# Optimization experiments

Hardware: AMD Instinct MI355X
Metric: run time of the kernel (lower is better)

Reference implementation:

```python
import jax, jax.numpy as jnp
import numpy as np

L_MODES = 64
GRID = 128
OUT_GRID = 128
CIN = 64
COUT = 64
T_DIM = 256


def legendre_table(L, theta):
    """Fully-normalized associated Legendre P_bar_l^m(cos(theta)), Condon-Shortley.
    Returns (L, 2L-1, n_theta) with m indexed -(L-1)..(L-1) at axis 1."""
    nt = theta.shape[0]
    x = np.cos(theta)
    s = np.sin(theta)
    P = np.zeros((L, L, nt))
    P[0, 0] = np.sqrt(1.0 / (4.0 * np.pi))
    for m in range(1, L):
        P[m, m] = -np.sqrt((2.0 * m + 1.0) / (2.0 * m)) * s * P[m - 1, m - 1]
    for m in range(L - 1):
        P[m + 1, m] = np.sqrt(2.0 * m + 3.0) * x * P[m, m]
    for m in range(L):
        for l in range(m + 2, L):
            a = np.sqrt((4.0 * l * l - 1.0) / (l * l - m * m))
            b = np.sqrt(((l - 1.0) ** 2 - m * m) / (4.0 * (l - 1.0) ** 2 - 1.0))
            P[l, m] = a * (x * P[l - 1, m] - b * P[l - 2, m])
    T = np.zeros((L, 2 * L - 1, nt))
    for m in range(L):
        T[:, L - 1 + m, :] = P[:, m, :]
        if m > 0:
            T[:, L - 1 - m, :] = ((-1.0) ** m) * P[:, m, :]
    return T.astype(np.float32)


def setup_inputs() -> dict:
    key = jax.random.key(0)
    ks = jax.random.split(key, 8)
    theta = np.pi * (np.arange(GRID) + 0.5) / GRID
    theta_out = np.pi * (np.arange(OUT_GRID) + 0.5) / OUT_GRID
    P_in = jnp.asarray(legendre_table(L_MODES, theta))            # (L, 2L-1, GRID)
    P_out = jnp.asarray(legendre_table(L_MODES, theta_out))       # (L, 2L-1, OUT_GRID)
    quad_w = jnp.asarray((np.pi / GRID) * np.sin(theta), dtype=jnp.float32)
    scale_w = 1.0 / (CIN + COUT)
    return {
        "x": jax.random.normal(ks[0], (GRID, GRID, CIN), jnp.float32),
        "t_emb": jax.random.normal(ks[1], (T_DIM,), jnp.float32),
        "wr": scale_w * jax.random.normal(ks[2], (L_MODES, 2 * L_MODES - 1, CIN, COUT), jnp.float32),
        "wi": scale_w * jax.random.normal(ks[3], (L_MODES, 2 * L_MODES - 1, CIN, COUT), jnp.float32),
        "conv_w": jax.random.normal(ks[4], (CIN, COUT), jnp.float32) / np.sqrt(CIN),
        "conv_b": jnp.zeros((COUT,), jnp.float32),
        "time_w": jax.random.normal(ks[5], (COUT, COUT), jnp.float32),
        "dense_w": jax.random.normal(ks[6], (T_DIM, 2 * COUT), jnp.float32) / np.sqrt(T_DIM),
        "ln_scale": jnp.ones((COUT,), jnp.float32),
        "ln_bias": jnp.zeros((COUT,), jnp.float32),
        "P_in": P_in,
        "P_out": P_out,
        "quad_w": quad_w,
    }


def reference(x, t_emb, wr, wi, conv_w, conv_b, time_w, dense_w, ln_scale, ln_bias, P_in, P_out, quad_w):
    L = P_in.shape[0]
    G_out = P_out.shape[2]
    nlon = x.shape[1]
    m_idx = np.arange(-(L - 1), L)

    # ---- forward spherical harmonic transform (lon FFT + Legendre quadrature) ----
    f = jnp.fft.fft(x.astype(jnp.complex64), axis=1) * (2.0 * np.pi / nlon)  # (nlat, nlon, Cin)
    fm = f[:, np.mod(m_idx, nlon), :] * quad_w[:, None, None]                # (nlat, 2L-1, Cin)
    flm = jnp.einsum('tmc,lmt->lmc', fm, P_in)                                # (L, 2L-1, Cin)

    # ---- per-(l,m) complex spectral conv ----
    w = wr + 1j * wi
    flm = jnp.einsum('lmi,lmio->lmo', flm, w)                                 # (L, 2L-1, Cout)

    # ---- inverse SHT onto output grid ----
    g = jnp.einsum('lmo,lmt->tmo', flm, P_out)                                # (G_out, 2L-1, Cout)
    phi = 2.0 * np.pi * np.arange(G_out) / G_out
    E = jnp.asarray(np.exp(1j * np.outer(m_idx, phi)).astype(np.complex64))   # (2L-1, G_out)
    x_spec = jnp.real(jnp.einsum('tmo,mk->tko', g, E))                        # (G_out, G_out, Cout)

    # ---- residual time-conditioned path (TimeConv2D, einsum as written in source) ----
    h = jnp.einsum('lmk,ko->lmo', x, conv_w) + conv_b                          # 1x1 conv
    psi = t_emb @ dense_w
    w_t, b_t = jnp.split(psi, 2, axis=-1)
    h = jnp.einsum('ij,j,lmk->lmi', time_w, w_t, h) + b_t[None, None, :]
    h = jax.image.resize(h, (G_out, G_out, h.shape[-1]), method='bicubic')

    # ---- add, layernorm over channels, relu ----
    out = x_spec + h
    mu = jnp.mean(out, axis=-1, keepdims=True)
    var = jnp.var(out, axis=-1, keepdims=True)
    out = (out - mu) * jax.lax.rsqrt(var + 1e-6) * ln_scale + ln_bias
    return jax.nn.relu(out)
```

## Files before the change

### kernel.cpp

```cpp
#include <hip/hip_runtime.h>
#include <math.h>

#define LM 64
#define MM 127
#define GG 128
#define CC 64
#define OO 64

#define TWO_PI 6.28318530717958647692f

__global__ __launch_bounds__(256) void k_dft(const float* __restrict__ x,
                                             const float* __restrict__ quad_w,
                                             const float* __restrict__ conv_w,
                                             const float* __restrict__ conv_b,
                                             const float* __restrict__ t_emb,
                                             const float* __restrict__ dense_w,
                                             const float* __restrict__ time_w,
                                             float2* __restrict__ F,
                                             float* __restrict__ Sv,
                                             float* __restrict__ aux) {
    int b = blockIdx.x;
    int tx = threadIdx.x;

    if (b == 512) {
        __shared__ float psis[128];
        if (tx < 128) {
            float acc = 0.f;
            for (int tq = 0; tq < 256; ++tq) acc += t_emb[tq] * dense_w[tq * 128 + tx];
            psis[tx] = acc;
            aux[tx] = acc;
        }
        __syncthreads();
        if (tx < 64) {
            float tv = 0.f;
            for (int q = 0; q < 64; ++q) tv += time_w[tx * 64 + q] * psis[q];
            aux[128 + tx] = tv;
        }
        return;
    }

    int t = b >> 2, cq = b & 3;
    int c0base = cq * 16;

    __shared__ __align__(16) float xs[GG * 16];
    __shared__ float2 tab[GG];
    __shared__ float cwsl[16];
    __shared__ float Sp[2][GG];
    __shared__ float bsum_s;

    {
        const float* xp = x + (size_t)t * GG * CC + c0base;
        for (int idx = tx; idx < GG * 16 / 4; idx += 256) {
            int n = idx >> 2, c4 = idx & 3;
            *(float4*)&xs[n * 16 + c4 * 4] = *(const float4*)&xp[n * CC + c4 * 4];
        }
    }
    if (tx < GG) {
        float ang = (TWO_PI / GG) * tx;
        tab[tx] = make_float2(cosf(ang), sinf(ang));
    }
    if (tx >= 128 && tx < 144) {
        int c = c0base + (tx - 128);
        float s = 0.f;
        for (int o = 0; o < OO; ++o) s += conv_w[c * OO + o];
        cwsl[tx - 128] = s;
    }
    if (tx == 144) {
        float bs = 0.f;
        for (int o = 0; o < OO; ++o) bs += conv_b[o];
        bsum_s = bs;
    }
    __syncthreads();

    int k = tx & 63, cg = tx >> 6;
    int c0 = cg * 4;

    float sr[4], si[4];
#pragma unroll
    for (int j = 0; j < 4; ++j) { sr[j] = 0.f; si[j] = 0.f; }

    int kn = 0;
#pragma unroll 4
    for (int n = 0; n < GG; ++n) {
        float2 w = tab[kn];
        const float4 v = *(const float4*)&xs[n * 16 + c0];
        float vv[4] = {v.x, v.y, v.z, v.w};
#pragma unroll
        for (int j = 0; j < 4; ++j) {
            sr[j] += vv[j] * w.x;
            si[j] -= vv[j] * w.y;
        }
        kn = (kn + k) & (GG - 1);
    }
    float sc = (TWO_PI / GG) * quad_w[t];

    {
        float2* Fp = F + ((size_t)t * 64 + k) * CC + c0base + c0;
        *(float4*)&Fp[0] = make_float4(sr[0] * sc, si[0] * sc, sr[1] * sc, si[1] * sc);
        *(float4*)&Fp[2] = make_float4(sr[2] * sc, si[2] * sc, sr[3] * sc, si[3] * sc);
    }

    {
        int n2 = tx & 127, h = tx >> 7;
        float p = 0.f;
#pragma unroll
        for (int j = 0; j < 8; ++j) p += xs[n2 * 16 + h * 8 + j] * cwsl[h * 8 + j];
        Sp[h][n2] = p;
    }
    __syncthreads();
    if (tx < GG) {
        float v = Sp[0][tx] + Sp[1][tx] + (cq == 0 ? bsum_s : 0.f);
        Sv[(size_t)cq * GG * GG + t * GG + tx] = v;
    }
}

__global__ __launch_bounds__(256) void k_leg_fwd(const float2* __restrict__ F,
                                                 const float* __restrict__ P_in,
                                                 float2* __restrict__ flmp) {
    int m = blockIdx.x;
    int lh = blockIdx.y;
    int tq = blockIdx.z;
    int l0 = lh * 32;
    if (l0 + 31 < m) return;
    int t0 = tq * 32;

    __shared__ __align__(16) float2 Fs[32 * 64];
    __shared__ __align__(16) float  Ps[32 * 36];
    int tx = threadIdx.x;
    int c = tx & 63, lg = tx >> 6;

    for (int idx = tx; idx < 32 * 32; idx += 256) {
        int lr = idx >> 5, tl = idx & 31;
        Ps[tl * 36 + lr] = P_in[((size_t)(l0 + lr) * MM + 63 + m) * GG + t0 + tl];
    }
    for (int idx = tx; idx < 32 * 64; idx += 256) {
        int tl = idx >> 6, cc = idx & 63;
        Fs[idx] = F[((size_t)(t0 + tl) * 64 + m) * CC + cc];
    }
    __syncthreads();

    float sr[8], si[8];
#pragma unroll
    for (int j = 0; j < 8; ++j) { sr[j] = 0.f; si[j] = 0.f; }

#pragma unroll 2
    for (int tl = 0; tl < 32; ++tl) {
        float2 f = Fs[tl * 64 + c];
        const float* pp = &Ps[tl * 36 + lg * 8];
        float4 p0 = *(const float4*)pp;
        float4 p1 = *(const float4*)(pp + 4);
        float pv[8] = {p0.x, p0.y, p0.z, p0.w, p1.x, p1.y, p1.z, p1.w};
#pragma unroll
        for (int j = 0; j < 8; ++j) {
            sr[j] += f.x * pv[j];
            si[j] += f.y * pv[j];
        }
    }
#pragma unroll
    for (int j = 0; j < 8; ++j) {
        int l = l0 + lg * 8 + j;
        if (l >= m)
            flmp[(((size_t)tq * 64 + l) * 64 + m) * CC + c] = make_float2(sr[j], si[j]);
    }
}

__global__ __launch_bounds__(256) void k_wmul(const float2* __restrict__ flmp,
                                              const float* __restrict__ wr,
                                              const float* __restrict__ wi,
                                              float2* __restrict__ flm2) {
    int l = blockIdx.x, mi = blockIdx.y;
    int m = mi - 63;
    int am = m < 0 ? -m : m;
    if (l < am) return;
    __shared__ float2 fs[CC];
    __shared__ float2 part[16][CC];
    int tx = threadIdx.x, ol = tx & 15, ig = tx >> 4;
    if (tx < 64) {
        float2 f = make_float2(0.f, 0.f);
#pragma unroll
        for (int q = 0; q < 4; ++q) {
            float2 v = flmp[(((size_t)q * 64 + l) * 64 + am) * CC + tx];
            f.x += v.x;
            f.y += v.y;
        }
        if (m < 0) {
            float sgn = (am & 1) ? -1.f : 1.f;
            f.x *= sgn;
            f.y *= -sgn;
        }
        fs[tx] = f;
    }
    __syncthreads();
    size_t base = ((size_t)(l * MM + mi) * CC) * OO;
    const float4* wr4 = (const float4*)(wr + base);
    const float4* wi4 = (const float4*)(wi + base);
    float ar[4] = {0.f, 0.f, 0.f, 0.f}, ai[4] = {0.f, 0.f, 0.f, 0.f};
#pragma unroll
    for (int di = 0; di < 4; ++di) {
        int i = ig * 4 + di;
        float4 a = wr4[i * 16 + ol];
        float4 b = wi4[i * 16 + ol];
        float2 f = fs[i];
        ar[0] += f.x * a.x - f.y * b.x;  ai[0] += f.x * b.x + f.y * a.x;
        ar[1] += f.x * a.y - f.y * b.y;  ai[1] += f.x * b.y + f.y * a.y;
        ar[2] += f.x * a.z - f.y * b.z;  ai[2] += f.x * b.z + f.y * a.z;
        ar[3] += f.x * a.w - f.y * b.w;  ai[3] += f.x * b.w + f.y * a.w;
    }
#pragma unroll
    for (int j = 0; j < 4; ++j) part[ig][ol * 4 + j] = make_float2(ar[j], ai[j]);
    __syncthreads();
    if (tx < 64) {
        float rr = 0.f, ri = 0.f;
#pragma unroll
        for (int q = 0; q < 16; ++q) {
            float2 p = part[q][tx];
            rr += p.x;
            ri += p.y;
        }
        flm2[(size_t)(l * MM + mi) * OO + tx] = make_float2(rr, ri);
    }
}

__global__ __launch_bounds__(256) void k_leg_inv(const float2* __restrict__ flm2,
                                                 const float* __restrict__ P_out,
                                                 float2* __restrict__ g) {
    int mi = blockIdx.x;
    int th = blockIdx.y >> 1, oh = blockIdx.y & 1;
    int t0 = th * 32, o0 = oh * 32;

    __shared__ __align__(16) float2 Ws[64 * 32];
    __shared__ __align__(16) float  Ps[64 * 32];
    int tx = threadIdx.x;
    int ol = tx & 31, tg = tx >> 5;
    int o = o0 + ol;

    for (int idx = tx; idx < 64 * 32; idx += 256) {
        int ls = idx >> 5, oo = idx & 31;
        Ws[idx] = flm2[(size_t)(ls * MM + mi) * OO + o0 + oo];
    }
    for (int idx = tx; idx < 64 * 32; idx += 256) {
        int ls = idx >> 5, tt = idx & 31;
        Ps[idx] = P_out[((size_t)ls * MM + mi) * GG + t0 + tt];
    }
    __syncthreads();

    float gr[4], gi[4];
#pragma unroll
    for (int j = 0; j < 4; ++j) { gr[j] = 0.f; gi[j] = 0.f; }

#pragma unroll 2
    for (int l = 0; l < 64; ++l) {
        float2 wv = Ws[l * 32 + ol];
        const float4 p = *(const float4*)&Ps[l * 32 + tg * 4];
        float pv[4] = {p.x, p.y, p.z, p.w};
#pragma unroll
        for (int j = 0; j < 4; ++j) {
            gr[j] += wv.x * pv[j];
            gi[j] += wv.y * pv[j];
        }
    }
#pragma unroll
    for (int j = 0; j < 4; ++j) {
        int t = t0 + tg * 4 + j;
        g[((size_t)t * MM + mi) * OO + o] = make_float2(gr[j], gi[j]);
    }
}

__global__ __launch_bounds__(512) void k_final(const float2* __restrict__ g,
                                               const float* __restrict__ Sv,
                                               const float* __restrict__ aux,
                                               const float* __restrict__ ln_scale,
                                               const float* __restrict__ ln_bias,
                                               float* __restrict__ out) {
    __shared__ float2 gs[64 * 64];
    __shared__ float Ss[64];
    int t = blockIdx.x, kh = blockIdx.y;
    int tx = threadIdx.x;
    int o = tx & 63, kg = tx >> 6;

    if (tx < 64) {
        float s = 0.f;
#pragma unroll
        for (int q = 0; q < 4; ++q) s += Sv[(size_t)q * GG * GG + t * GG + kh * 64 + tx];
        Ss[tx] = s;
    }

    float zr[8], zi[8], accr[8], acci[8];
#pragma unroll
    for (int j = 0; j < 8; ++j) {
        int k = kh * 64 + kg * 8 + j;
        float phi = (TWO_PI / GG) * k;
        float s, c;
        sincosf(phi, &s, &c);
        zr[j] = c; zi[j] = s;
        accr[j] = 0.f; acci[j] = 0.f;
    }

    for (int pass = 0; pass < 2; ++pass) {
        int mbase = (pass == 0) ? 64 : 0;
        int cnt = (pass == 0) ? 63 : 64;
        __syncthreads();
        for (int idx = tx; idx < cnt * 64; idx += 512) {
            int mm = idx >> 6, oo = idx & 63;
            gs[idx] = g[((size_t)t * MM + mbase + mm) * OO + oo];
        }
        __syncthreads();
        for (int mm = cnt - 1; mm >= 0; --mm) {
            float2 gv = gs[mm * 64 + o];
#pragma unroll
            for (int j = 0; j < 8; ++j) {
                float tr = accr[j] * zr[j] - acci[j] * zi[j] + gv.x;
                float ti = accr[j] * zi[j] + acci[j] * zr[j] + gv.y;
                accr[j] = tr; acci[j] = ti;
            }
        }
    }

    float tvec = aux[128 + o], bt = aux[64 + o];
    float lns = ln_scale[o], lnb = ln_bias[o];
#pragma unroll
    for (int j = 0; j < 8; ++j) {
        int k = kh * 64 + kg * 8 + j;
        float sgn = (k & 1) ? -1.f : 1.f;
        float xsp = sgn * (accr[j] * zr[j] - acci[j] * zi[j]);
        float val = xsp + tvec * Ss[k - kh * 64] + bt;

        float mu = val;
#pragma unroll
        for (int off = 1; off < 64; off <<= 1) mu += __shfl_xor(mu, off);
        mu *= (1.f / 64.f);
        float d = val - mu;
        float var = d * d;
#pragma unroll
        for (int off = 1; off < 64; off <<= 1) var += __shfl_xor(var, off);
        var *= (1.f / 64.f);
        float r = d * rsqrtf(var + 1e-6f) * lns + lnb;
        out[((size_t)(t * GG) + k) * OO + o] = fmaxf(r, 0.f);
    }
}

extern "C" void kernel_launch(void* const* d_in, const int* in_sizes, int n_in,
                              void* d_out, int out_size, void* d_ws, size_t ws_size,
                              hipStream_t stream) {
    const float* x        = (const float*)d_in[0];
    const float* t_emb    = (const float*)d_in[1];
    const float* wr       = (const float*)d_in[2];
    const float* wi       = (const float*)d_in[3];
    const float* conv_w   = (const float*)d_in[4];
    const float* conv_b   = (const float*)d_in[5];
    const float* time_w   = (const float*)d_in[6];
    const float* dense_w  = (const float*)d_in[7];
    const float* ln_scale = (const float*)d_in[8];
    const float* ln_bias  = (const float*)d_in[9];
    const float* P_in     = (const float*)d_in[10];
    const float* P_out    = (const float*)d_in[11];
    const float* quad_w   = (const float*)d_in[12];

    float* ws = (float*)d_ws;
    float*  aux  = ws;
    float2* F    = (float2*)(ws + 512);
    float2* flmp = (float2*)(ws + 1049088);
    float2* flm2 = (float2*)(ws + 3146240);
    float2* g    = (float2*)(ws + 4186624);
    float*  Sv   = ws + 6267392;

    float* out = (float*)d_out;

    k_dft<<<513, 256, 0, stream>>>(x, quad_w, conv_w, conv_b, t_emb, dense_w, time_w,
                                   F, Sv, aux);
    k_leg_fwd<<<dim3(64, 2, 4), 256, 0, stream>>>(F, P_in, flmp);
    k_wmul<<<dim3(LM, MM), 256, 0, stream>>>(flmp, wr, wi, flm2);
    k_leg_inv<<<dim3(MM, 8), 256, 0, stream>>>(flm2, P_out, g);
    k_final<<<dim3(GG, 2), 512, 0, stream>>>(g, Sv, aux, ln_scale, ln_bias, out);
}
```

Measured before the change: 325.5 us.

## Fuse five stage kernels into one cooperative persistent kernel with grid syncs

Merges the DFT, forward Legendre, weight multiply, inverse Legendre and final layernorm kernels into one cooperative kernel of 512 blocks separated by grid.sync, with a shared-memory union reused across stages. Stages that had more or fewer blocks now use grid-stride loops, and the final stage is remapped to 256 threads per block over quarter k-ranges. The aim is to remove the per-launch overhead and the gaps between the five launches. The cost is serialized grid barriers, a fixed grid size that leaves large stages such as the weight multiply to loop, and a reduced thread count in the final stage. Skipped weight-multiply tiles now write explicit zeros, which the previous version did not do.

```diff
diff --git a/kernel.cpp b/kernel.cpp
--- a/kernel.cpp
+++ b/kernel.cpp
@@ -1,341 +1,334 @@
 #include <hip/hip_runtime.h>
+#include <hip/hip_cooperative_groups.h>
 #include <math.h>
+
+namespace cg = cooperative_groups;
 
 #define LM 64
 #define MM 127
 #define GG 128
 #define CC 64
 #define OO 64
+#define NBLK 512
 
 #define TWO_PI 6.28318530717958647692f
 
-__global__ __launch_bounds__(256) void k_dft(const float* __restrict__ x,
-                                             const float* __restrict__ quad_w,
-                                             const float* __restrict__ conv_w,
-                                             const float* __restrict__ conv_b,
-                                             const float* __restrict__ t_emb,
-                                             const float* __restrict__ dense_w,
-                                             const float* __restrict__ time_w,
-                                             float2* __restrict__ F,
-                                             float* __restrict__ Sv,
-                                             float* __restrict__ aux) {
+__global__ __launch_bounds__(256, 2) void k_fused(
+    const float* __restrict__ x, const float* __restrict__ t_emb,
+    const float* __restrict__ wr, const float* __restrict__ wi,
+    const float* __restrict__ conv_w, const float* __restrict__ conv_b,
+    const float* __restrict__ time_w, const float* __restrict__ dense_w,
+    const float* __restrict__ ln_scale, const float* __restrict__ ln_bias,
+    const float* __restrict__ P_in, const float* __restrict__ P_out,
+    const float* __restrict__ quad_w,
+    float2* __restrict__ F, float2* __restrict__ flmp,
+    float2* __restrict__ flm2, float2* __restrict__ g,
+    float* __restrict__ Sv, float* __restrict__ aux,
+    float* __restrict__ out)
+{
+    cg::grid_group grid = cg::this_grid();
     int b = blockIdx.x;
     int tx = threadIdx.x;
 
-    if (b == 512) {
-        __shared__ float psis[128];
-        if (tx < 128) {
-            float acc = 0.f;
-            for (int tq = 0; tq < 256; ++tq) acc += t_emb[tq] * dense_w[tq * 128 + tx];
-            psis[tx] = acc;
-            aux[tx] = acc;
-        }
-        __syncthreads();
-        if (tx < 64) {
-            float tv = 0.f;
-            for (int q = 0; q < 64; ++q) tv += time_w[tx * 64 + q] * psis[q];
-            aux[128 + tx] = tv;
-        }
-        return;
-    }
-
-    int t = b >> 2, cq = b & 3;
-    int c0base = cq * 16;
-
-    __shared__ __align__(16) float xs[GG * 16];
-    __shared__ float2 tab[GG];
-    __shared__ float cwsl[16];
-    __shared__ float Sp[2][GG];
-    __shared__ float bsum_s;
+    __shared__ __align__(16) union {
+        struct { float xs[GG * 16]; float2 tab[GG]; float cwsl[16];
+                 float Sp[2][GG]; float bsum; } p1;
+        float psis[128];
+        struct { float2 Fs[32 * 64]; float Ps[32 * 36]; } p2;
+        struct { float2 fs[CC]; float2 part[16][CC]; } p3;
+        struct { float2 Ws[64 * 32]; float Ps[64 * 32]; } p4;
+        struct { float2 gs[64 * 64]; float Ss[32]; } p5;
+    } u;
 
     {
+        int t = b >> 2, cq = b & 3;
+        int c0base = cq * 16;
+
         const float* xp = x + (size_t)t * GG * CC + c0base;
         for (int idx = tx; idx < GG * 16 / 4; idx += 256) {
             int n = idx >> 2, c4 = idx & 3;
-            *(float4*)&xs[n * 16 + c4 * 4] = *(const float4*)&xp[n * CC + c4 * 4];
-        }
-    }
-    if (tx < GG) {
-        float ang = (TWO_PI / GG) * tx;
-        tab[tx] = make_float2(cosf(ang), sinf(ang));
-    }
-    if (tx >= 128 && tx < 144) {
-        int c = c0base + (tx - 128);
-        float s = 0.f;
-        for (int o = 0; o < OO; ++o) s += conv_w[c * OO + o];
-        cwsl[tx - 128] = s;
-    }
-    if (tx == 144) {
-        float bs = 0.f;
-        for (int o = 0; o < OO; ++o) bs += conv_b[o];
-        bsum_s = bs;
-    }
-    __syncthreads();
-
-    int k = tx & 63, cg = tx >> 6;
-    int c0 = cg * 4;
-
-    float sr[4], si[4];
-#pragma unroll
-    for (int j = 0; j < 4; ++j) { sr[j] = 0.f; si[j] = 0.f; }
-
-    int kn = 0;
+            *(float4*)&u.p1.xs[n * 16 + c4 * 4] = *(const float4*)&xp[n * CC + c4 * 4];
+        }
+        if (tx < GG) {
+            float ang = (TWO_PI / GG) * tx;
+            u.p1.tab[tx] = make_float2(cosf(ang), sinf(ang));
+        }
+        if (tx >= 128 && tx < 144) {
+            int c = c0base + (tx - 128);
+            float s = 0.f;
+            for (int o = 0; o < OO; ++o) s += conv_w[c * OO + o];
+            u.p1.cwsl[tx - 128] = s;
+        }
+        if (tx == 144) {
+            float bs = 0.f;
+            for (int o = 0; o < OO; ++o) bs += conv_b[o];
+            u.p1.bsum = bs;
+        }
+        __syncthreads();
+
+        int k = tx & 63, cgrp = tx >> 6;
+        int c0 = cgrp * 4;
+
+        float sr[4], si[4];
+#pragma unroll
+        for (int j = 0; j < 4; ++j) { sr[j] = 0.f; si[j] = 0.f; }
+
+        int kn = 0;
 #pragma unroll 4
-    for (int n = 0; n < GG; ++n) {
-        float2 w = tab[kn];
-        const float4 v = *(const float4*)&xs[n * 16 + c0];
-        float vv[4] = {v.x, v.y, v.z, v.w};
+        for (int n = 0; n < GG; ++n) {
+            float2 w = u.p1.tab[kn];
+            const float4 v = *(const float4*)&u.p1.xs[n * 16 + c0];
+            float vv[4] = {v.x, v.y, v.z, v.w};
+#pragma unroll
+            for (int j = 0; j < 4; ++j) {
+                sr[j] += vv[j] * w.x;
+                si[j] -= vv[j] * w.y;
+            }
+            kn = (kn + k) & (GG - 1);
+        }
+        float sc = (TWO_PI / GG) * quad_w[t];
+        {
+            float2* Fp = F + ((size_t)t * 64 + k) * CC + c0base + c0;
+            *(float4*)&Fp[0] = make_float4(sr[0] * sc, si[0] * sc, sr[1] * sc, si[1] * sc);
+            *(float4*)&Fp[2] = make_float4(sr[2] * sc, si[2] * sc, sr[3] * sc, si[3] * sc);
+        }
+
+        {
+            int n2 = tx & 127, h = tx >> 7;
+            float p = 0.f;
+#pragma unroll
+            for (int j = 0; j < 8; ++j) p += u.p1.xs[n2 * 16 + h * 8 + j] * u.p1.cwsl[h * 8 + j];
+            u.p1.Sp[h][n2] = p;
+        }
+        __syncthreads();
+        if (tx < GG) {
+            float v = u.p1.Sp[0][tx] + u.p1.Sp[1][tx] + (cq == 0 ? u.p1.bsum : 0.f);
+            Sv[(size_t)cq * GG * GG + t * GG + tx] = v;
+        }
+
+        if (b == 0) {
+            __syncthreads();
+            if (tx < 128) {
+                float acc = 0.f;
+                for (int tq = 0; tq < 256; ++tq) acc += t_emb[tq] * dense_w[tq * 128 + tx];
+                u.psis[tx] = acc;
+                aux[tx] = acc;
+            }
+            __syncthreads();
+            if (tx < 64) {
+                float tv = 0.f;
+                for (int q = 0; q < 64; ++q) tv += time_w[tx * 64 + q] * u.psis[q];
+                aux[128 + tx] = tv;
+            }
+        }
+    }
+    grid.sync();
+
+    {
+        int m = b & 63, lh = (b >> 6) & 1, tq = b >> 7;
+        int l0 = lh * 32, t0 = tq * 32;
+        if (l0 + 31 >= m) {
+            int c = tx & 63, lg = tx >> 6;
+
+            for (int idx = tx; idx < 32 * 32; idx += 256) {
+                int lr = idx >> 5, tl = idx & 31;
+                u.p2.Ps[tl * 36 + lr] = P_in[((size_t)(l0 + lr) * MM + 63 + m) * GG + t0 + tl];
+            }
+            for (int idx = tx; idx < 32 * 64; idx += 256) {
+                int tl = idx >> 6, cc = idx & 63;
+                u.p2.Fs[idx] = F[((size_t)(t0 + tl) * 64 + m) * CC + cc];
+            }
+            __syncthreads();
+
+            float sr[8], si[8];
+#pragma unroll
+            for (int j = 0; j < 8; ++j) { sr[j] = 0.f; si[j] = 0.f; }
+
+#pragma unroll 2
+            for (int tl = 0; tl < 32; ++tl) {
+                float2 f = u.p2.Fs[tl * 64 + c];
+                const float* pp = &u.p2.Ps[tl * 36 + lg * 8];
+                float4 p0 = *(const float4*)pp;
+                float4 p1 = *(const float4*)(pp + 4);
+                float pv[8] = {p0.x, p0.y, p0.z, p0.w, p1.x, p1.y, p1.z, p1.w};
+#pragma unroll
+                for (int j = 0; j < 8; ++j) {
+                    sr[j] += f.x * pv[j];
+                    si[j] += f.y * pv[j];
+                }
+            }
+#pragma unroll
+            for (int j = 0; j < 8; ++j) {
+                int l = l0 + lg * 8 + j;
+                if (l >= m)
+                    flmp[(((size_t)tq * 64 + l) * 64 + m) * CC + c] = make_float2(sr[j], si[j]);
+            }
+        }
+    }
+    grid.sync();
+
+    for (int tt = b; tt < 64 * MM; tt += NBLK) {
+        int l = tt / MM, mi = tt % MM;
+        int m = mi - 63;
+        int am = m < 0 ? -m : m;
+        if (l < am) {
+            if (tx < 64) flm2[(size_t)(l * MM + mi) * OO + tx] = make_float2(0.f, 0.f);
+            continue;
+        }
+        int ol = tx & 15, ig = tx >> 4;
+        if (tx < 64) {
+            float2 f = make_float2(0.f, 0.f);
+#pragma unroll
+            for (int q = 0; q < 4; ++q) {
+                float2 v = flmp[(((size_t)q * 64 + l) * 64 + am) * CC + tx];
+                f.x += v.x;
+                f.y += v.y;
+            }
+            if (m < 0) {
+                float sgn = (am & 1) ? -1.f : 1.f;
+                f.x *= sgn;
+                f.y *= -sgn;
+            }
+            u.p3.fs[tx] = f;
+        }
+        __syncthreads();
+        size_t base = ((size_t)(l * MM + mi) * CC) * OO;
+        const float4* wr4 = (const float4*)(wr + base);
+        const float4* wi4 = (const float4*)(wi + base);
+        float ar[4] = {0.f, 0.f, 0.f, 0.f}, ai[4] = {0.f, 0.f, 0.f, 0.f};
+#pragma unroll
+        for (int di = 0; di < 4; ++di) {
+            int i = ig * 4 + di;
+            float4 a = wr4[i * 16 + ol];
+            float4 bb = wi4[i * 16 + ol];
+            float2 f = u.p3.fs[i];
+            ar[0] += f.x * a.x - f.y * bb.x;  ai[0] += f.x * bb.x + f.y * a.x;
+            ar[1] += f.x * a.y - f.y * bb.y;  ai[1] += f.x * bb.y + f.y * a.y;
+            ar[2] += f.x * a.z - f.y * bb.z;  ai[2] += f.x * bb.z + f.y * a.z;
+            ar[3] += f.x * a.w - f.y * bb.w;  ai[3] += f.x * bb.w + f.y * a.w;
+        }
+#pragma unroll
+        for (int j = 0; j < 4; ++j) u.p3.part[ig][ol * 4 + j] = make_float2(ar[j], ai[j]);
+        __syncthreads();
+        if (tx < 64) {
+            float rr = 0.f, ri = 0.f;
+#pragma unroll
+            for (int q = 0; q < 16; ++q) {
+                float2 p = u.p3.part[q][tx];
+                rr += p.x;
+                ri += p.y;
+            }
+            flm2[(size_t)(l * MM + mi) * OO + tx] = make_float2(rr, ri);
+        }
+        __syncthreads();
+    }
+    grid.sync();
+
+    for (int tt = b; tt < MM * 8; tt += NBLK) {
+        int mi = tt % MM, y = tt / MM;
+        int th = y >> 1, oh = y & 1;
+        int t0 = th * 32, o0 = oh * 32;
+        int ol = tx & 31, tg = tx >> 5;
+        int o = o0 + ol;
+
+        __syncthreads();
+        for (int idx = tx; idx < 64 * 32; idx += 256) {
+            int ls = idx >> 5, oo = idx & 31;
+            u.p4.Ws[idx] = flm2[(size_t)(ls * MM + mi) * OO + o0 + oo];
+        }
+        for (int idx = tx; idx < 64 * 32; idx += 256) {
+            int ls = idx >> 5, t2 = idx & 31;
+            u.p4.Ps[idx] = P_out[((size_t)ls * MM + mi) * GG + t0 + t2];
+        }
+        __syncthreads();
+
+        float gr[4], gi[4];
+#pragma unroll
+        for (int j = 0; j < 4; ++j) { gr[j] = 0.f; gi[j] = 0.f; }
+
+#pragma unroll 2
+        for (int l = 0; l < 64; ++l) {
+            float2 wv = u.p4.Ws[l * 32 + ol];
+            const float4 p = *(const float4*)&u.p4.Ps[l * 32 + tg * 4];
+            float pv[4] = {p.x, p.y, p.z, p.w};
+#pragma unroll
+            for (int j = 0; j < 4; ++j) {
+                gr[j] += wv.x * pv[j];
+                gi[j] += wv.y * pv[j];
+            }
+        }
 #pragma unroll
         for (int j = 0; j < 4; ++j) {
-            sr[j] += vv[j] * w.x;
-            si[j] -= vv[j] * w.y;
-        }
-        kn = (kn + k) & (GG - 1);
-    }
-    float sc = (TWO_PI / GG) * quad_w[t];
+            int t = t0 + tg * 4 + j;
+            g[((size_t)t * MM + mi) * OO + o] = make_float2(gr[j], gi[j]);
+        }
+    }
+    grid.sync();
 
     {
-        float2* Fp = F + ((size_t)t * 64 + k) * CC + c0base + c0;
-        *(float4*)&Fp[0] = make_float4(sr[0] * sc, si[0] * sc, sr[1] * sc, si[1] * sc);
-        *(float4*)&Fp[2] = make_float4(sr[2] * sc, si[2] * sc, sr[3] * sc, si[3] * sc);
-    }
-
-    {
-        int n2 = tx & 127, h = tx >> 7;
-        float p = 0.f;
-#pragma unroll
-        for (int j = 0; j < 8; ++j) p += xs[n2 * 16 + h * 8 + j] * cwsl[h * 8 + j];
-        Sp[h][n2] = p;
-    }
-    __syncthreads();
-    if (tx < GG) {
-        float v = Sp[0][tx] + Sp[1][tx] + (cq == 0 ? bsum_s : 0.f);
-        Sv[(size_t)cq * GG * GG + t * GG + tx] = v;
-    }
-}
-
-__global__ __launch_bounds__(256) void k_leg_fwd(const float2* __restrict__ F,
-                                                 const float* __restrict__ P_in,
-                                                 float2* __restrict__ flmp) {
-    int m = blockIdx.x;
-    int lh = blockIdx.y;
-    int tq = blockIdx.z;
-    int l0 = lh * 32;
-    if (l0 + 31 < m) return;
-    int t0 = tq * 32;
-
-    __shared__ __align__(16) float2 Fs[32 * 64];
-    __shared__ __align__(16) float  Ps[32 * 36];
-    int tx = threadIdx.x;
-    int c = tx & 63, lg = tx >> 6;
-
-    for (int idx = tx; idx < 32 * 32; idx += 256) {
-        int lr = idx >> 5, tl = idx & 31;
-        Ps[tl * 36 + lr] = P_in[((size_t)(l0 + lr) * MM + 63 + m) * GG + t0 + tl];
-    }
-    for (int idx = tx; idx < 32 * 64; idx += 256) {
-        int tl = idx >> 6, cc = idx & 63;
-        Fs[idx] = F[((size_t)(t0 + tl) * 64 + m) * CC + cc];
-    }
-    __syncthreads();
-
-    float sr[8], si[8];
-#pragma unroll
-    for (int j = 0; j < 8; ++j) { sr[j] = 0.f; si[j] = 0.f; }
-
-#pragma unroll 2
-    for (int tl = 0; tl < 32; ++tl) {
-        float2 f = Fs[tl * 64 + c];
-        const float* pp = &Ps[tl * 36 + lg * 8];
-        float4 p0 = *(const float4*)pp;
-        float4 p1 = *(const float4*)(pp + 4);
-        float pv[8] = {p0.x, p0.y, p0.z, p0.w, p1.x, p1.y, p1.z, p1.w};
+        int t = b >> 2, kq = b & 3;
+        int o = tx & 63, kg = tx >> 6;
+
+        if (tx < 32) {
+            float s = 0.f;
+#pragma unroll
+            for (int q = 0; q < 4; ++q)
+                s += Sv[(size_t)q * GG * GG + t * GG + kq * 32 + tx];
+            u.p5.Ss[tx] = s;
+        }
+
+        float zr[8], zi[8], accr[8], acci[8];
 #pragma unroll
         for (int j = 0; j < 8; ++j) {
-            sr[j] += f.x * pv[j];
-            si[j] += f.y * pv[j];
-        }
-    }
-#pragma unroll
-    for (int j = 0; j < 8; ++j) {
-        int l = l0 + lg * 8 + j;
-        if (l >= m)
-            flmp[(((size_t)tq * 64 + l) * 64 + m) * CC + c] = make_float2(sr[j], si[j]);
-    }
-}
-
-__global__ __launch_bounds__(256) void k_wmul(const float2* __restrict__ flmp,
-                                              const float* __restrict__ wr,
-                                              const float* __restrict__ wi,
-                                              float2* __restrict__ flm2) {
-    int l = blockIdx.x, mi = blockIdx.y;
-    int m = mi - 63;
-    int am = m < 0 ? -m : m;
-    if (l < am) return;
-    __shared__ float2 fs[CC];
-    __shared__ float2 part[16][CC];
-    int tx = threadIdx.x, ol = tx & 15, ig = tx >> 4;
-    if (tx < 64) {
-        float2 f = make_float2(0.f, 0.f);
-#pragma unroll
-        for (int q = 0; q < 4; ++q) {
-            float2 v = flmp[(((size_t)q * 64 + l) * 64 + am) * CC + tx];
-            f.x += v.x;
-            f.y += v.y;
-        }
-        if (m < 0) {
-            float sgn = (am & 1) ? -1.f : 1.f;
-            f.x *= sgn;
-            f.y *= -sgn;
-        }
-        fs[tx] = f;
-    }
-    __syncthreads();
-    size_t base = ((size_t)(l * MM + mi) * CC) * OO;
-    const float4* wr4 = (const float4*)(wr + base);
-    const float4* wi4 = (const float4*)(wi + base);
-    float ar[4] = {0.f, 0.f, 0.f, 0.f}, ai[4] = {0.f, 0.f, 0.f, 0.f};
-#pragma unroll
-    for (int di = 0; di < 4; ++di) {
-        int i = ig * 4 + di;
-        float4 a = wr4[i * 16 + ol];
-        float4 b = wi4[i * 16 + ol];
-        float2 f = fs[i];
-        ar[0] += f.x * a.x - f.y * b.x;  ai[0] += f.x * b.x + f.y * a.x;
-        ar[1] += f.x * a.y - f.y * b.y;  ai[1] += f.x * b.y + f.y * a.y;
-        ar[2] += f.x * a.z - f.y * b.z;  ai[2] += f.x * b.z + f.y * a.z;
-        ar[3] += f.x * a.w - f.y * b.w;  ai[3] += f.x * b.w + f.y * a.w;
-    }
-#pragma unroll
-    for (int j = 0; j < 4; ++j) part[ig][ol * 4 + j] = make_float2(ar[j], ai[j]);
-    __syncthreads();
-    if (tx < 64) {
-        float rr = 0.f, ri = 0.f;
-#pragma unroll
-        for (int q = 0; q < 16; ++q) {
-            float2 p = part[q][tx];
-            rr += p.x;
-            ri += p.y;
-        }
-        flm2[(size_t)(l * MM + mi) * OO + tx] = make_float2(rr, ri);
-    }
-}
-
-__global__ __launch_bounds__(256) void k_leg_inv(const float2* __restrict__ flm2,
-                                                 const float* __restrict__ P_out,
-                                                 float2* __restrict__ g) {
-    int mi = blockIdx.x;
-    int th = blockIdx.y >> 1, oh = blockIdx.y & 1;
-    int t0 = th * 32, o0 = oh * 32;
-
-    __shared__ __align__(16) float2 Ws[64 * 32];
-    __shared__ __align__(16) float  Ps[64 * 32];
-    int tx = threadIdx.x;
-    int ol = tx & 31, tg = tx >> 5;
-    int o = o0 + ol;
-
-    for (int idx = tx; idx < 64 * 32; idx += 256) {
-        int ls = idx >> 5, oo = idx & 31;
-        Ws[idx] = flm2[(size_t)(ls * MM + mi) * OO + o0 + oo];
-    }
-    for (int idx = tx; idx < 64 * 32; idx += 256) {
-        int ls = idx >> 5, tt = idx & 31;
-        Ps[idx] = P_out[((size_t)ls * MM + mi) * GG + t0 + tt];
-    }
-    __syncthreads();
-
-    float gr[4], gi[4];
-#pragma unroll
-    for (int j = 0; j < 4; ++j) { gr[j] = 0.f; gi[j] = 0.f; }
-
-#pragma unroll 2
-    for (int l = 0; l < 64; ++l) {
-        float2 wv = Ws[l * 32 + ol];
-        const float4 p = *(const float4*)&Ps[l * 32 + tg * 4];
-        float pv[4] = {p.x, p.y, p.z, p.w};
-#pragma unroll
-        for (int j = 0; j < 4; ++j) {
-            gr[j] += wv.x * pv[j];
-            gi[j] += wv.y * pv[j];
-        }
-    }
-#pragma unroll
-    for (int j = 0; j < 4; ++j) {
-        int t = t0 + tg * 4 + j;
-        g[((size_t)t * MM + mi) * OO + o] = make_float2(gr[j], gi[j]);
-    }
-}
-
-__global__ __launch_bounds__(512) void k_final(const float2* __restrict__ g,
-                                               const float* __restrict__ Sv,
-                                               const float* __restrict__ aux,
-                                               const float* __restrict__ ln_scale,
-                                               const float* __restrict__ ln_bias,
-                                               float* __restrict__ out) {
-    __shared__ float2 gs[64 * 64];
-    __shared__ float Ss[64];
-    int t = blockIdx.x, kh = blockIdx.y;
-    int tx = threadIdx.x;
-    int o = tx & 63, kg = tx >> 6;
-
-    if (tx < 64) {
-        float s = 0.f;
-#pragma unroll
-        for (int q = 0; q < 4; ++q) s += Sv[(size_t)q * GG * GG + t * GG + kh * 64 + tx];
-        Ss[tx] = s;
-    }
-
-    float zr[8], zi[8], accr[8], acci[8];
-#pragma unroll
-    for (int j = 0; j < 8; ++j) {
-        int k = kh * 64 + kg * 8 + j;
-        float phi = (TWO_PI / GG) * k;
-        float s, c;
-        sincosf(phi, &s, &c);
-        zr[j] = c; zi[j] = s;
-        accr[j] = 0.f; acci[j] = 0.f;
-    }
-
-    for (int pass = 0; pass < 2; ++pass) {
-        int mbase = (pass == 0) ? 64 : 0;
-        int cnt = (pass == 0) ? 63 : 64;
-        __syncthreads();
-        for (int idx = tx; idx < cnt * 64; idx += 512) {
-            int mm = idx >> 6, oo = idx & 63;
-            gs[idx] = g[((size_t)t * MM + mbase + mm) * OO + oo];
-        }
-        __syncthreads();
-        for (int mm = cnt - 1; mm >= 0; --mm) {
-            float2 gv = gs[mm * 64 + o];
-#pragma unroll
-            for (int j = 0; j < 8; ++j) {
-                float tr = accr[j] * zr[j] - acci[j] * zi[j] + gv.x;
-                float ti = accr[j] * zi[j] + acci[j] * zr[j] + gv.y;
-                accr[j] = tr; acci[j] = ti;
-            }
-        }
-    }
-
-    float tvec = aux[128 + o], bt = aux[64 + o];
-    float lns = ln_scale[o], lnb = ln_bias[o];
-#pragma unroll
-    for (int j = 0; j < 8; ++j) {
-        int k = kh * 64 + kg * 8 + j;
-        float sgn = (k & 1) ? -1.f : 1.f;
-        float xsp = sgn * (accr[j] * zr[j] - acci[j] * zi[j]);
-        float val = xsp + tvec * Ss[k - kh * 64] + bt;
-
-        float mu = val;
-#pragma unroll
-        for (int off = 1; off < 64; off <<= 1) mu += __shfl_xor(mu, off);
-        mu *= (1.f / 64.f);
-        float d = val - mu;
-        float var = d * d;
-#pragma unroll
-        for (int off = 1; off < 64; off <<= 1) var += __shfl_xor(var, off);
-        var *= (1.f / 64.f);
-        float r = d * rsqrtf(var + 1e-6f) * lns + lnb;
-        out[((size_t)(t * GG) + k) * OO + o] = fmaxf(r, 0.f);
+            int k = kq * 32 + kg * 8 + j;
+            float phi = (TWO_PI / GG) * k;
+            float s, c;
+            sincosf(phi, &s, &c);
+            zr[j] = c; zi[j] = s;
+            accr[j] = 0.f; acci[j] = 0.f;
+        }
+
+        for (int pass = 0; pass < 2; ++pass) {
+            int mbase = (pass == 0) ? 64 : 0;
+            int cnt = (pass == 0) ? 63 : 64;
+            __syncthreads();
+            for (int idx = tx; idx < cnt * 64; idx += 256) {
+                int mm = idx >> 6, oo = idx & 63;
+                u.p5.gs[idx] = g[((size_t)t * MM + mbase + mm) * OO + oo];
+            }
+            __syncthreads();
+            for (int mm = cnt - 1; mm >= 0; --mm) {
+                float2 gv = u.p5.gs[mm * 64 + o];
+#pragma unroll
+                for (int j = 0; j < 8; ++j) {
+                    float tr = accr[j] * zr[j] - acci[j] * zi[j] + gv.x;
+                    float ti = accr[j] * zi[j] + acci[j] * zr[j] + gv.y;
+                    accr[j] = tr; acci[j] = ti;
+                }
+            }
+        }
+
+        float tvec = aux[128 + o], bt = aux[64 + o];
+        float lns = ln_scale[o], lnb = ln_bias[o];
+#pragma unroll
+        for (int j = 0; j < 8; ++j) {
+            int k = kq * 32 + kg * 8 + j;
+            float sgn = (k & 1) ? -1.f : 1.f;
+            float xsp = sgn * (accr[j] * zr[j] - acci[j] * zi[j]);
+            float val = xsp + tvec * u.p5.Ss[kg * 8 + j] + bt;
+
+            float mu = val;
+#pragma unroll
+            for (int off = 1; off < 64; off <<= 1) mu += __shfl_xor(mu, off);
+            mu *= (1.f / 64.f);
+            float d = val - mu;
+            float var = d * d;
+#pragma unroll
+            for (int off = 1; off < 64; off <<= 1) var += __shfl_xor(var, off);
+            var *= (1.f / 64.f);
+            float r = d * rsqrtf(var + 1e-6f) * lns + lnb;
+            out[((size_t)(t * GG) + k) * OO + o] = fmaxf(r, 0.f);
+        }
     }
 }
 
@@ -364,12 +357,12 @@
     float2* g    = (float2*)(ws + 4186624);
     float*  Sv   = ws + 6267392;
 
-    float* out = (float*)d_out;
-
-    k_dft<<<513, 256, 0, stream>>>(x, quad_w, conv_w, conv_b, t_emb, dense_w, time_w,
-                                   F, Sv, aux);
-    k_leg_fwd<<<dim3(64, 2, 4), 256, 0, stream>>>(F, P_in, flmp);
-    k_wmul<<<dim3(LM, MM), 256, 0, stream>>>(flmp, wr, wi, flm2);
-    k_leg_inv<<<dim3(MM, 8), 256, 0, stream>>>(flm2, P_out, g);
-    k_final<<<dim3(GG, 2), 512, 0, stream>>>(g, Sv, aux, ln_scale, ln_bias, out);
+    float* outp = (float*)d_out;
+
+    void* args[] = {(void*)&x, (void*)&t_emb, (void*)&wr, (void*)&wi,
+                    (void*)&conv_w, (void*)&conv_b, (void*)&time_w, (void*)&dense_w,
+                    (void*)&ln_scale, (void*)&ln_bias, (void*)&P_in, (void*)&P_out,
+                    (void*)&quad_w, (void*)&F, (void*)&flmp, (void*)&flm2,
+                    (void*)&g, (void*)&Sv, (void*)&aux, (void*)&outp};
+    hipLaunchCooperativeKernel((void*)k_fused, dim3(NBLK), dim3(256), args, 0, stream);
 }
```

After: 585.4 us. 1.8x slower.

## Map each (l,m) weight multiply to one wavefront using readlane broadcast

Applied to the files above, without the earlier changes.

Restructures the spectral weight-multiply kernel so each 64-lane wavefront handles one (l,m) pair: each lane owns one output channel and loops over all input channels, broadcasting the input coefficient with readlane instead of shared memory. This removes the shared-memory staging, two block barriers and the 16-way partial-sum reduction, and packs four (l,m) pairs per block. It also writes zeros explicitly for invalid l<|m| entries instead of leaving them unwritten. Weight loads become scalar floats rather than float4, which may reduce load width, and the kernel stays bound by streaming the large weight tensors.

```diff
diff --git a/kernel.cpp b/kernel.cpp
--- a/kernel.cpp
+++ b/kernel.cpp
@@ -168,57 +168,46 @@
                                               const float* __restrict__ wr,
                                               const float* __restrict__ wi,
                                               float2* __restrict__ flm2) {
-    int l = blockIdx.x, mi = blockIdx.y;
+    int wv = threadIdx.x >> 6;
+    int lane = threadIdx.x & 63;
+    int tt = blockIdx.x * 4 + wv;
+    if (tt >= 64 * MM) return;
+    int l = tt / MM, mi = tt % MM;
     int m = mi - 63;
     int am = m < 0 ? -m : m;
-    if (l < am) return;
-    __shared__ float2 fs[CC];
-    __shared__ float2 part[16][CC];
-    int tx = threadIdx.x, ol = tx & 15, ig = tx >> 4;
-    if (tx < 64) {
-        float2 f = make_float2(0.f, 0.f);
-#pragma unroll
-        for (int q = 0; q < 4; ++q) {
-            float2 v = flmp[(((size_t)q * 64 + l) * 64 + am) * CC + tx];
-            f.x += v.x;
-            f.y += v.y;
-        }
-        if (m < 0) {
-            float sgn = (am & 1) ? -1.f : 1.f;
-            f.x *= sgn;
-            f.y *= -sgn;
-        }
-        fs[tx] = f;
-    }
-    __syncthreads();
+    size_t obase = (size_t)(l * MM + mi) * OO;
+    if (l < am) {
+        flm2[obase + lane] = make_float2(0.f, 0.f);
+        return;
+    }
+
+    float fx = 0.f, fy = 0.f;
+#pragma unroll
+    for (int q = 0; q < 4; ++q) {
+        float2 v = flmp[(((size_t)q * 64 + l) * 64 + am) * CC + lane];
+        fx += v.x;
+        fy += v.y;
+    }
+    if (m < 0) {
+        float sgn = (am & 1) ? -1.f : 1.f;
+        fx *= sgn;
+        fy *= -sgn;
+    }
+
     size_t base = ((size_t)(l * MM + mi) * CC) * OO;
-    const float4* wr4 = (const float4*)(wr + base);
-    const float4* wi4 = (const float4*)(wi + base);
-    float ar[4] = {0.f, 0.f, 0.f, 0.f}, ai[4] = {0.f, 0.f, 0.f, 0.f};
-#pragma unroll
-    for (int di = 0; di < 4; ++di) {
-        int i = ig * 4 + di;
-        float4 a = wr4[i * 16 + ol];
-        float4 b = wi4[i * 16 + ol];
-        float2 f = fs[i];
-        ar[0] += f.x * a.x - f.y * b.x;  ai[0] += f.x * b.x + f.y * a.x;
-        ar[1] += f.x * a.y - f.y * b.y;  ai[1] += f.x * b.y + f.y * a.y;
-        ar[2] += f.x * a.z - f.y * b.z;  ai[2] += f.x * b.z + f.y * a.z;
-        ar[3] += f.x * a.w - f.y * b.w;  ai[3] += f.x * b.w + f.y * a.w;
-    }
-#pragma unroll
-    for (int j = 0; j < 4; ++j) part[ig][ol * 4 + j] = make_float2(ar[j], ai[j]);
-    __syncthreads();
-    if (tx < 64) {
-        float rr = 0.f, ri = 0.f;
-#pragma unroll
-        for (int q = 0; q < 16; ++q) {
-            float2 p = part[q][tx];
-            rr += p.x;
-            ri += p.y;
-        }
-        flm2[(size_t)(l * MM + mi) * OO + tx] = make_float2(rr, ri);
-    }
+    const float* wrp = wr + base;
+    const float* wip = wi + base;
+    float ar = 0.f, ai = 0.f;
+#pragma unroll
+    for (int i = 0; i < CC; ++i) {
+        float fxi = __uint_as_float(__builtin_amdgcn_readlane(__float_as_uint(fx), i));
+        float fyi = __uint_as_float(__builtin_amdgcn_readlane(__float_as_uint(fy), i));
+        float a = wrp[i * OO + lane];
+        float bv = wip[i * OO + lane];
+        ar += fxi * a - fyi * bv;
+        ai += fxi * bv + fyi * a;
+    }
+    flm2[obase + lane] = make_float2(ar, ai);
 }
 
 __global__ __launch_bounds__(256) void k_leg_inv(const float2* __restrict__ flm2,
@@ -369,7 +358,7 @@
     k_dft<<<513, 256, 0, stream>>>(x, quad_w, conv_w, conv_b, t_emb, dense_w, time_w,
                                    F, Sv, aux);
     k_leg_fwd<<<dim3(64, 2, 4), 256, 0, stream>>>(F, P_in, flmp);
-    k_wmul<<<dim3(LM, MM), 256, 0, stream>>>(flmp, wr, wi, flm2);
+    k_wmul<<<(64 * MM + 3) / 4, 256, 0, stream>>>(flmp, wr, wi, flm2);
     k_leg_inv<<<dim3(MM, 8), 256, 0, stream>>>(flm2, P_out, g);
     k_final<<<dim3(GG, 2), 512, 0, stream>>>(g, Sv, aux, ln_scale, ln_bias, out);
 }
```

After: 334.6 us. +2.8%, slower.
